# Kernel tuning notes

Measured on AMD Instinct MI355X. Metric: run time of the kernel, lower is better.

## Reference

```python
import jax, jax.numpy as jnp
import numpy as np

B, LAT, HID, N, H = 16, 128, 256, 256, 4
C = HID // H
TAU = 1.0


def setup_inputs() -> dict:
    key = jax.random.key(0)
    ks = jax.random.split(key, 16)
    g = lambda k, shape: (jax.random.normal(k, shape, dtype=jnp.float32) * 0.05)
    u = jax.random.uniform(ks[15], (B, N, N), dtype=jnp.float32, minval=1e-6, maxval=1.0 - 1e-6)
    gumbel = -jnp.log(-jnp.log(u))
    return {
        "x": jax.random.normal(ks[0], (B, LAT), dtype=jnp.float32),
        "W0": g(ks[1], (LAT, HID)), "b0": g(ks[2], (HID,)),
        "W1": g(ks[3], (HID, HID)), "b1": g(ks[4], (HID,)),
        "W2": g(ks[5], (HID, N * HID)), "b2": g(ks[6], (N * HID,)),
        "Wg": g(ks[7], (HID, H * C)),
        "att_src": g(ks[8], (H, C)), "att_dst": g(ks[9], (H, C)),
        "bg": g(ks[10], (H * C,)),
        "Wl": g(ks[11], (HID, N)), "bl": g(ks[12], (N,)),
        "gumbel": gumbel,
    }


def _forward(x, W0, b0, W1, b1, W2, b2, Wg, att_src, att_dst, bg, Wl, bl, gumbel):
    batch = x.shape[0]
    n = bl.shape[0]
    heads, ch = att_src.shape
    hid = heads * ch
    # MLP: latent -> hidden -> hidden -> n_nodes*hidden
    h = jax.nn.relu(x @ W0 + b0)
    h = jax.nn.relu(h @ W1 + b1)
    h = (h @ W2 + b2).reshape(batch, n, hid)
    # edge list: torch.combinations (i<j) directed src->dst, plus PyG self-loops
    s_np, d_np = np.triu_indices(n, k=1)
    src = jnp.concatenate([jnp.asarray(s_np, dtype=jnp.int32), jnp.arange(n, dtype=jnp.int32)])
    dst = jnp.concatenate([jnp.asarray(d_np, dtype=jnp.int32), jnp.arange(n, dtype=jnp.int32)])

    def gat(xn):  # xn: [N, hid]
        gfeat = (xn @ Wg).reshape(n, heads, ch)
        a_s = jnp.einsum('nhc,hc->nh', gfeat, att_src)
        a_d = jnp.einsum('nhc,hc->nh', gfeat, att_dst)
        e = jax.nn.leaky_relu(a_s[src] + a_d[dst], 0.2)          # [E, H]
        m = jax.lax.stop_gradient(jax.ops.segment_max(e, dst, num_segments=n))
        p = jnp.exp(e - m[dst])
        denom = jax.ops.segment_sum(p, dst, num_segments=n)
        alpha = p / denom[dst]                                   # segment softmax per dst
        out = jax.ops.segment_sum(gfeat[src] * alpha[:, :, None], dst, num_segments=n)
        return out.reshape(n, hid) + bg

    h = jax.nn.elu(jax.vmap(gat)(h))  # dropout is a no-op (eval mode)
    logits = h @ Wl + bl
    # gumbel_softmax(hard=True) with straight-through estimator
    y_soft = jax.nn.softmax((logits + gumbel) / TAU, axis=-1)
    y_hard = jax.nn.one_hot(jnp.argmax(y_soft, axis=-1), n, dtype=y_soft.dtype)
    y = jax.lax.stop_gradient(y_hard - y_soft) + y_soft
    adj = jnp.clip(y + jnp.swapaxes(y, 1, 2), 0.0, 1.0)
    return adj


def reference(x, W0, b0, W1, b1, W2, b2, Wg, att_src, att_dst, bg, Wl, bl, gumbel):
    return _forward(x, W0, b0, W1, b1, W2, b2, Wg, att_src, att_dst, bg, Wl, bl, gumbel)
```

## Files before the change

### kernel.cpp

```cpp
#include <hip/hip_runtime.h>
#include <math.h>

#define NB 16
#define LAT 128
#define HID 256
#define NN 256
#define NH 4
#define JT 4

__device__ __forceinline__ float lrelu02(float x){ return x > 0.f ? x : 0.2f*x; }
__device__ __forceinline__ float eluf(float x){ return x > 0.f ? x : expm1f(x); }

__global__ __launch_bounds__(256) void k_mlp12(const float* __restrict__ x,
    const float* __restrict__ W0, const float* __restrict__ b0,
    const float* __restrict__ W1, const float* __restrict__ b1,
    float* __restrict__ h2)
{
    __shared__ float xs[LAT];
    __shared__ float h1s[HID];
    int b = blockIdx.x, t = threadIdx.x;
    if (t < LAT) xs[t] = x[b*LAT + t];
    __syncthreads();
    float acc = b0[t];
    for (int k = 0; k < LAT; ++k) acc = fmaf(xs[k], W0[k*HID + t], acc);
    h1s[t] = fmaxf(acc, 0.f);
    __syncthreads();
    float acc2 = b1[t];
    for (int k = 0; k < HID; ++k) acc2 = fmaf(h1s[k], W1[k*HID + t], acc2);
    h2[b*HID + t] = fmaxf(acc2, 0.f);
}

__global__ __launch_bounds__(512) void k_mlp3g(
    const float* __restrict__ h2, const float* __restrict__ W2,
    const float* __restrict__ b2, const float* __restrict__ Wg,
    const float* __restrict__ att_src, const float* __restrict__ att_dst,
    float* __restrict__ gfeat, float* __restrict__ a_s, float* __restrict__ a_d)
{
    __shared__ float h2T[HID][16];
    __shared__ float red[256*17];
    __shared__ float h3s[NB][HID+1];
    int t = threadIdx.x;
    int n = blockIdx.x;
    int col = t & 255, kh = t >> 8;
    for (int idx = t; idx < NB*HID; idx += 512) {
        int b = idx & 15, k = idx >> 4;
        h2T[k][b] = h2[b*HID + k];
    }
    __syncthreads();
    float acc[NB];
    #pragma unroll
    for (int b = 0; b < NB; ++b) acc[b] = 0.f;
    const float* w2p = W2 + (size_t)kh*128*65536 + (size_t)n*HID + col;
    for (int k0 = 0; k0 < 128; k0 += 16) {
        float wv[16];
        #pragma unroll
        for (int u = 0; u < 16; ++u) wv[u] = w2p[(size_t)(k0+u)*65536];
        #pragma unroll
        for (int u = 0; u < 16; ++u) {
            const float* hr = &h2T[kh*128 + k0 + u][0];
            #pragma unroll
            for (int b = 0; b < NB; ++b) acc[b] = fmaf(hr[b], wv[u], acc[b]);
        }
    }
    if (kh == 1) {
        #pragma unroll
        for (int b = 0; b < NB; ++b) red[col*17 + b] = acc[b];
    }
    __syncthreads();
    if (kh == 0) {
        float bv = b2[n*HID + col];
        #pragma unroll
        for (int b = 0; b < NB; ++b) h3s[b][col] = acc[b] + red[col*17 + b] + bv;
    }
    __syncthreads();
    int l = t & 63, w = t >> 6, cb = l*4;
    float4 g[2];
    g[0] = make_float4(0.f,0.f,0.f,0.f); g[1] = g[0];
    #pragma unroll 4
    for (int k = 0; k < HID; ++k) {
        float4 wg = *(const float4*)&Wg[k*HID + cb];
        #pragma unroll
        for (int rr = 0; rr < 2; ++rr) {
            float hv = h3s[w*2+rr][k];
            g[rr].x = fmaf(hv, wg.x, g[rr].x);
            g[rr].y = fmaf(hv, wg.y, g[rr].y);
            g[rr].z = fmaf(hv, wg.z, g[rr].z);
            g[rr].w = fmaf(hv, wg.w, g[rr].w);
        }
    }
    float4 s4 = *(const float4*)&att_src[cb];
    float4 d4 = *(const float4*)&att_dst[cb];
    int h = l >> 4;
    #pragma unroll
    for (int rr = 0; rr < 2; ++rr) {
        int b = w*2 + rr;
        *(float4*)&gfeat[b*(NN*HID) + n*HID + cb] = g[rr];
        float ps = g[rr].x*s4.x + g[rr].y*s4.y + g[rr].z*s4.z + g[rr].w*s4.w;
        float pd = g[rr].x*d4.x + g[rr].y*d4.y + g[rr].z*d4.z + g[rr].w*d4.w;
        #pragma unroll
        for (int off = 1; off < 16; off <<= 1) {
            ps += __shfl_xor(ps, off);
            pd += __shfl_xor(pd, off);
        }
        if ((l & 15) == 0) {
            a_s[b*(NN*NH) + n*NH + h] = ps;
            a_d[b*(NN*NH) + n*NH + h] = pd;
        }
    }
}

__global__ __launch_bounds__(256) void k_prefden(const float* __restrict__ a_s,
    const float* __restrict__ a_d, float* __restrict__ sArr)
{
    __shared__ float as_sh[NN];
    int id = blockIdx.x;
    int b = id >> 4, h = (id >> 2) & 3, jc = id & 3;
    int t = threadIdx.x;
    as_sh[t] = a_s[b*(NN*NH) + t*NH + h];
    __syncthreads();
    int jl = t >> 2, r = t & 3;
    int j = jc*64 + jl;
    float ad = a_d[b*(NN*NH) + j*NH + h];
    float lm = -INFINITY;
    for (int i = r; i <= j; i += 4) lm = fmaxf(lm, as_sh[i]);
    lm = fmaxf(lm, __shfl_xor(lm, 1));
    lm = fmaxf(lm, __shfl_xor(lm, 2));
    float m = lrelu02(lm + ad);
    float s = 0.f;
    for (int i = r; i <= j; i += 4) s += expf(lrelu02(as_sh[i] + ad) - m);
    s += __shfl_xor(s, 1);
    s += __shfl_xor(s, 2);
    if (r == 0) {
        sArr[b*(NN*NH) + j*NH + h] = expf(-m) / s;
    }
}

__global__ __launch_bounds__(256) void k_gatlog(
    const float* __restrict__ gfeat, const float* __restrict__ a_s,
    const float* __restrict__ a_d, const float* __restrict__ sArr,
    const float* __restrict__ bg, const float* __restrict__ Wl,
    const float* __restrict__ bl, const float* __restrict__ gumbel,
    int* __restrict__ biOut)
{
    __shared__ float pa[4*1032];
    __shared__ float part[16*256];
    __shared__ float houts[NN*4];
    __shared__ float redv[4][JT];
    __shared__ int   redi[4][JT];

    int t = threadIdx.x;
    int id = blockIdx.x;
    int xcd = id & 7, k2 = id >> 3;
    int bb = (xcd << 1) | (k2 >> 6);
    int j0 = (k2 & 63) * JT;
    int l = t & 63, w = t >> 6;

    float pr[JT][4];
    if (w*64 <= j0 + JT - 1) {
        float4 as4 = *(const float4*)&a_s[bb*(NN*NH) + t*NH];
        #pragma unroll
        for (int jj = 0; jj < JT; ++jj) {
            int j = j0 + jj;
            float4 ad4 = *(const float4*)&a_d[bb*(NN*NH) + j*NH];
            float4 sv4 = *(const float4*)&sArr[bb*(NN*NH) + j*NH];
            bool valid = (t <= j);
            pr[jj][0] = valid ? expf(lrelu02(as4.x+ad4.x)) * sv4.x : 0.f;
            pr[jj][1] = valid ? expf(lrelu02(as4.y+ad4.y)) * sv4.y : 0.f;
            pr[jj][2] = valid ? expf(lrelu02(as4.z+ad4.z)) * sv4.z : 0.f;
            pr[jj][3] = valid ? expf(lrelu02(as4.w+ad4.w)) * sv4.w : 0.f;
        }
    } else {
        #pragma unroll
        for (int jj = 0; jj < JT; ++jj)
            #pragma unroll
            for (int h = 0; h < 4; ++h) pr[jj][h] = 0.f;
    }
    #pragma unroll
    for (int h = 0; h < 4; ++h)
        *(float4*)&pa[h*1032 + t*4] = make_float4(pr[0][h], pr[1][h], pr[2][h], pr[3][h]);
    __syncthreads();

    int q = l >> 4, c4 = (l & 15) * 4;
    float4 aj[JT];
    #pragma unroll
    for (int jj = 0; jj < JT; ++jj) aj[jj] = make_float4(0.f,0.f,0.f,0.f);
    const float* gb = gfeat + bb*(NN*HID);
    int lim = j0 + JT - w*64; lim = lim < 0 ? 0 : (lim > 64 ? 64 : lim);
    #pragma unroll 4
    for (int ii = 0; ii < lim; ++ii) {
        int ig = w*64 + ii;
        float4 g4 = *(const float4*)&gb[ig*HID + q*64 + c4];
        float4 pv = *(const float4*)&pa[q*1032 + ig*4];
        aj[0].x = fmaf(pv.x, g4.x, aj[0].x); aj[0].y = fmaf(pv.x, g4.y, aj[0].y);
        aj[0].z = fmaf(pv.x, g4.z, aj[0].z); aj[0].w = fmaf(pv.x, g4.w, aj[0].w);
        aj[1].x = fmaf(pv.y, g4.x, aj[1].x); aj[1].y = fmaf(pv.y, g4.y, aj[1].y);
        aj[1].z = fmaf(pv.y, g4.z, aj[1].z); aj[1].w = fmaf(pv.y, g4.w, aj[1].w);
        aj[2].x = fmaf(pv.z, g4.x, aj[2].x); aj[2].y = fmaf(pv.z, g4.y, aj[2].y);
        aj[2].z = fmaf(pv.z, g4.z, aj[2].z); aj[2].w = fmaf(pv.z, g4.w, aj[2].w);
        aj[3].x = fmaf(pv.w, g4.x, aj[3].x); aj[3].y = fmaf(pv.w, g4.y, aj[3].y);
        aj[3].z = fmaf(pv.w, g4.z, aj[3].z); aj[3].w = fmaf(pv.w, g4.w, aj[3].w);
    }
    #pragma unroll
    for (int jj = 0; jj < JT; ++jj)
        *(float4*)&part[(w*JT + jj)*256 + q*64 + c4] = aj[jj];
    __syncthreads();

    {
        float bgv = bg[t];
        float hh[JT];
        #pragma unroll
        for (int jj = 0; jj < JT; ++jj) {
            float s = part[(0*JT+jj)*256 + t] + part[(1*JT+jj)*256 + t]
                    + part[(2*JT+jj)*256 + t] + part[(3*JT+jj)*256 + t] + bgv;
            hh[jj] = eluf(s);
        }
        *(float4*)&houts[t*4] = make_float4(hh[0], hh[1], hh[2], hh[3]);
    }
    __syncthreads();

    int cb = l*4;
    float4 lg[JT];
    #pragma unroll
    for (int jj = 0; jj < JT; ++jj) lg[jj] = make_float4(0.f,0.f,0.f,0.f);
    #pragma unroll 2
    for (int kk = 0; kk < 64; ++kk) {
        int k = w*64 + kk;
        float4 hv  = *(const float4*)&houts[k*4];
        float4 wl4 = *(const float4*)&Wl[k*HID + cb];
        lg[0].x = fmaf(hv.x, wl4.x, lg[0].x); lg[0].y = fmaf(hv.x, wl4.y, lg[0].y);
        lg[0].z = fmaf(hv.x, wl4.z, lg[0].z); lg[0].w = fmaf(hv.x, wl4.w, lg[0].w);
        lg[1].x = fmaf(hv.y, wl4.x, lg[1].x); lg[1].y = fmaf(hv.y, wl4.y, lg[1].y);
        lg[1].z = fmaf(hv.y, wl4.z, lg[1].z); lg[1].w = fmaf(hv.y, wl4.w, lg[1].w);
        lg[2].x = fmaf(hv.z, wl4.x, lg[2].x); lg[2].y = fmaf(hv.z, wl4.y, lg[2].y);
        lg[2].z = fmaf(hv.z, wl4.z, lg[2].z); lg[2].w = fmaf(hv.z, wl4.w, lg[2].w);
        lg[3].x = fmaf(hv.w, wl4.x, lg[3].x); lg[3].y = fmaf(hv.w, wl4.y, lg[3].y);
        lg[3].z = fmaf(hv.w, wl4.z, lg[3].z); lg[3].w = fmaf(hv.w, wl4.w, lg[3].w);
    }
    #pragma unroll
    for (int jj = 0; jj < JT; ++jj)
        *(float4*)&part[(w*JT + jj)*256 + cb] = lg[jj];
    __syncthreads();

    float blv = bl[t];
    #pragma unroll
    for (int jj = 0; jj < JT; ++jj) {
        float z = part[(0*JT+jj)*256 + t] + part[(1*JT+jj)*256 + t]
                + part[(2*JT+jj)*256 + t] + part[(3*JT+jj)*256 + t]
                + blv + gumbel[bb*(NN*NN) + (j0+jj)*NN + t];
        float bv = z; int bi_ = t;
        #pragma unroll
        for (int off = 1; off < 64; off <<= 1) {
            float ov = __shfl_xor(bv, off);
            int   oi = __shfl_xor(bi_, off);
            if (ov > bv || (ov == bv && oi < bi_)) { bv = ov; bi_ = oi; }
        }
        if (l == 0) { redv[w][jj] = bv; redi[w][jj] = bi_; }
    }
    __syncthreads();
    if (t < JT) {
        float bv = redv[0][t]; int bi_ = redi[0][t];
        #pragma unroll
        for (int ww = 1; ww < 4; ++ww)
            if (redv[ww][t] > bv) { bv = redv[ww][t]; bi_ = redi[ww][t]; }
        biOut[bb*NN + j0 + t] = bi_;
    }
}

__global__ __launch_bounds__(256) void k_adj(const int* __restrict__ bi,
    float* __restrict__ adj)
{
    int bb = blockIdx.x, t = threadIdx.x;
    float4* ap = (float4*)(adj + (size_t)bb*(NN*NN));
    float4 z = make_float4(0.f,0.f,0.f,0.f);
    for (int idx = t; idx < NN*NN/4; idx += 256) ap[idx] = z;
    __syncthreads();
    int b = bi[bb*NN + t];
    adj[(size_t)bb*(NN*NN) + t*NN + b] = 1.0f;
    adj[(size_t)bb*(NN*NN) + b*NN + t] = 1.0f;
}

extern "C" void kernel_launch(void* const* d_in, const int* in_sizes, int n_in,
                              void* d_out, int out_size, void* d_ws, size_t ws_size,
                              hipStream_t stream)
{
    const float* x       = (const float*)d_in[0];
    const float* W0      = (const float*)d_in[1];
    const float* b0      = (const float*)d_in[2];
    const float* W1      = (const float*)d_in[3];
    const float* b1      = (const float*)d_in[4];
    const float* W2      = (const float*)d_in[5];
    const float* b2      = (const float*)d_in[6];
    const float* Wg      = (const float*)d_in[7];
    const float* att_src = (const float*)d_in[8];
    const float* att_dst = (const float*)d_in[9];
    const float* bg      = (const float*)d_in[10];
    const float* Wl      = (const float*)d_in[11];
    const float* bl      = (const float*)d_in[12];
    const float* gumbel  = (const float*)d_in[13];

    float* ws     = (float*)d_ws;
    float* h2     = ws;
    float* a_s    = h2 + 4096;
    float* a_d    = a_s + 16384;
    float* sArr   = a_d + 16384;
    int*   biIdx  = (int*)(sArr + 16384);
    float* gfeat  = (float*)d_out;
    float* adj    = (float*)d_out;

    k_mlp12  <<<NB, 256, 0, stream>>>(x, W0, b0, W1, b1, h2);
    k_mlp3g  <<<NN, 512, 0, stream>>>(h2, W2, b2, Wg, att_src, att_dst, gfeat, a_s, a_d);
    k_prefden<<<256, 256, 0, stream>>>(a_s, a_d, sArr);
    k_gatlog <<<NB*64, 256, 0, stream>>>(gfeat, a_s, a_d, sArr, bg, Wl, bl, gumbel, biIdx);
    k_adj    <<<NB, 256, 0, stream>>>(biIdx, adj);
}
```

Before: 88.86 us.

## Split W2 GEMM into its own wide kernel and compute GAT features in place

The fused MLP-layer-3 plus GAT-projection kernel is split in two. The first, k_h3, runs 1024 blocks of 256 threads, each handling 64 output columns with a four-way K split and double-buffered W2 loads, so the 64 MB W2 stream gets more parallelism and more loads in flight. The second kernel reads h3 back from the output buffer and overwrites each node's slice in place with its GAT features. This adds one extra launch and a global round trip for h3 (about 4 MB) in exchange for better bandwidth use on the dominant W2 read.

```diff
diff --git a/kernel.cpp b/kernel.cpp
--- a/kernel.cpp
+++ b/kernel.cpp
@@ -30,62 +30,93 @@
     h2[b*HID + t] = fmaxf(acc2, 0.f);
 }
 
-__global__ __launch_bounds__(512) void k_mlp3g(
+#define FMA16(KK, WV) do { \
+    const float4* hq = (const float4*)&h2T[KK][0]; \
+    float4 q0 = hq[0], q1 = hq[1], q2 = hq[2], q3 = hq[3]; \
+    acc[0] = fmaf(q0.x,(WV),acc[0]);  acc[1] = fmaf(q0.y,(WV),acc[1]); \
+    acc[2] = fmaf(q0.z,(WV),acc[2]);  acc[3] = fmaf(q0.w,(WV),acc[3]); \
+    acc[4] = fmaf(q1.x,(WV),acc[4]);  acc[5] = fmaf(q1.y,(WV),acc[5]); \
+    acc[6] = fmaf(q1.z,(WV),acc[6]);  acc[7] = fmaf(q1.w,(WV),acc[7]); \
+    acc[8] = fmaf(q2.x,(WV),acc[8]);  acc[9] = fmaf(q2.y,(WV),acc[9]); \
+    acc[10]= fmaf(q2.z,(WV),acc[10]); acc[11]= fmaf(q2.w,(WV),acc[11]); \
+    acc[12]= fmaf(q3.x,(WV),acc[12]); acc[13]= fmaf(q3.y,(WV),acc[13]); \
+    acc[14]= fmaf(q3.z,(WV),acc[14]); acc[15]= fmaf(q3.w,(WV),acc[15]); \
+} while (0)
+
+__global__ __launch_bounds__(256) void k_h3(
     const float* __restrict__ h2, const float* __restrict__ W2,
-    const float* __restrict__ b2, const float* __restrict__ Wg,
+    const float* __restrict__ b2, float* __restrict__ h3)
+{
+    __shared__ float h2T[HID][16];
+    __shared__ float red[3][64][17];
+    int t = threadIdx.x;
+    int c = t & 63, kh = t >> 6;
+    int col = blockIdx.x*64 + c;
+    for (int idx = t; idx < NB*HID; idx += 256) {
+        int b = idx & 15, k = idx >> 4;
+        h2T[k][b] = h2[b*HID + k];
+    }
+    __syncthreads();
+    float acc[16];
+    #pragma unroll
+    for (int b = 0; b < 16; ++b) acc[b] = 0.f;
+    const float* p = W2 + (size_t)(kh*64)*65536 + col;
+    float wa[8], wb[8];
+    #pragma unroll
+    for (int u = 0; u < 8; ++u) wa[u] = p[(size_t)u*65536];
+    for (int k0 = 0; k0 < 64; k0 += 16) {
+        #pragma unroll
+        for (int u = 0; u < 8; ++u) wb[u] = p[(size_t)(k0+8+u)*65536];
+        #pragma unroll
+        for (int u = 0; u < 8; ++u) { int kk = kh*64 + k0 + u; FMA16(kk, wa[u]); }
+        if (k0 + 16 < 64) {
+            #pragma unroll
+            for (int u = 0; u < 8; ++u) wa[u] = p[(size_t)(k0+16+u)*65536];
+        }
+        #pragma unroll
+        for (int u = 0; u < 8; ++u) { int kk = kh*64 + k0 + 8 + u; FMA16(kk, wb[u]); }
+    }
+    if (kh > 0) {
+        #pragma unroll
+        for (int b = 0; b < 16; ++b) red[kh-1][c][b] = acc[b];
+    }
+    __syncthreads();
+    if (kh == 0) {
+        float bv = b2[col];
+        #pragma unroll
+        for (int b = 0; b < 16; ++b) {
+            float s = acc[b] + red[0][c][b] + red[1][c][b] + red[2][c][b] + bv;
+            h3[(size_t)b*65536 + col] = s;
+        }
+    }
+}
+
+__global__ __launch_bounds__(512) void k_gfeatB(
+    float* __restrict__ g, const float* __restrict__ Wg,
     const float* __restrict__ att_src, const float* __restrict__ att_dst,
-    float* __restrict__ gfeat, float* __restrict__ a_s, float* __restrict__ a_d)
-{
-    __shared__ float h2T[HID][16];
-    __shared__ float red[256*17];
+    float* __restrict__ a_s, float* __restrict__ a_d)
+{
     __shared__ float h3s[NB][HID+1];
     int t = threadIdx.x;
     int n = blockIdx.x;
-    int col = t & 255, kh = t >> 8;
     for (int idx = t; idx < NB*HID; idx += 512) {
-        int b = idx & 15, k = idx >> 4;
-        h2T[k][b] = h2[b*HID + k];
-    }
-    __syncthreads();
-    float acc[NB];
-    #pragma unroll
-    for (int b = 0; b < NB; ++b) acc[b] = 0.f;
-    const float* w2p = W2 + (size_t)kh*128*65536 + (size_t)n*HID + col;
-    for (int k0 = 0; k0 < 128; k0 += 16) {
-        float wv[16];
-        #pragma unroll
-        for (int u = 0; u < 16; ++u) wv[u] = w2p[(size_t)(k0+u)*65536];
-        #pragma unroll
-        for (int u = 0; u < 16; ++u) {
-            const float* hr = &h2T[kh*128 + k0 + u][0];
-            #pragma unroll
-            for (int b = 0; b < NB; ++b) acc[b] = fmaf(hr[b], wv[u], acc[b]);
-        }
-    }
-    if (kh == 1) {
-        #pragma unroll
-        for (int b = 0; b < NB; ++b) red[col*17 + b] = acc[b];
-    }
-    __syncthreads();
-    if (kh == 0) {
-        float bv = b2[n*HID + col];
-        #pragma unroll
-        for (int b = 0; b < NB; ++b) h3s[b][col] = acc[b] + red[col*17 + b] + bv;
+        int b = idx >> 8, c = idx & 255;
+        h3s[b][c] = g[(size_t)b*65536 + n*HID + c];
     }
     __syncthreads();
     int l = t & 63, w = t >> 6, cb = l*4;
-    float4 g[2];
-    g[0] = make_float4(0.f,0.f,0.f,0.f); g[1] = g[0];
+    float4 gg[2];
+    gg[0] = make_float4(0.f,0.f,0.f,0.f); gg[1] = gg[0];
     #pragma unroll 4
     for (int k = 0; k < HID; ++k) {
         float4 wg = *(const float4*)&Wg[k*HID + cb];
         #pragma unroll
         for (int rr = 0; rr < 2; ++rr) {
             float hv = h3s[w*2+rr][k];
-            g[rr].x = fmaf(hv, wg.x, g[rr].x);
-            g[rr].y = fmaf(hv, wg.y, g[rr].y);
-            g[rr].z = fmaf(hv, wg.z, g[rr].z);
-            g[rr].w = fmaf(hv, wg.w, g[rr].w);
+            gg[rr].x = fmaf(hv, wg.x, gg[rr].x);
+            gg[rr].y = fmaf(hv, wg.y, gg[rr].y);
+            gg[rr].z = fmaf(hv, wg.z, gg[rr].z);
+            gg[rr].w = fmaf(hv, wg.w, gg[rr].w);
         }
     }
     float4 s4 = *(const float4*)&att_src[cb];
@@ -94,9 +125,9 @@
     #pragma unroll
     for (int rr = 0; rr < 2; ++rr) {
         int b = w*2 + rr;
-        *(float4*)&gfeat[b*(NN*HID) + n*HID + cb] = g[rr];
-        float ps = g[rr].x*s4.x + g[rr].y*s4.y + g[rr].z*s4.z + g[rr].w*s4.w;
-        float pd = g[rr].x*d4.x + g[rr].y*d4.y + g[rr].z*d4.z + g[rr].w*d4.w;
+        *(float4*)&g[(size_t)b*65536 + n*HID + cb] = gg[rr];
+        float ps = gg[rr].x*s4.x + gg[rr].y*s4.y + gg[rr].z*s4.z + gg[rr].w*s4.w;
+        float pd = gg[rr].x*d4.x + gg[rr].y*d4.y + gg[rr].z*d4.z + gg[rr].w*d4.w;
         #pragma unroll
         for (int off = 1; off < 16; off <<= 1) {
             ps += __shfl_xor(ps, off);
@@ -184,12 +215,12 @@
     float4 aj[JT];
     #pragma unroll
     for (int jj = 0; jj < JT; ++jj) aj[jj] = make_float4(0.f,0.f,0.f,0.f);
-    const float* gb = gfeat + bb*(NN*HID);
+    const float* gb = gfeat + (size_t)0;
     int lim = j0 + JT - w*64; lim = lim < 0 ? 0 : (lim > 64 ? 64 : lim);
     #pragma unroll 4
     for (int ii = 0; ii < lim; ++ii) {
         int ig = w*64 + ii;
-        float4 g4 = *(const float4*)&gb[ig*HID + q*64 + c4];
+        float4 g4 = *(const float4*)&gb[(size_t)bb*(NN*HID) + ig*HID + q*64 + c4];
         float4 pv = *(const float4*)&pa[q*1032 + ig*4];
         aj[0].x = fmaf(pv.x, g4.x, aj[0].x); aj[0].y = fmaf(pv.x, g4.y, aj[0].y);
         aj[0].z = fmaf(pv.x, g4.z, aj[0].z); aj[0].w = fmaf(pv.x, g4.w, aj[0].w);
@@ -246,7 +277,7 @@
     for (int jj = 0; jj < JT; ++jj) {
         float z = part[(0*JT+jj)*256 + t] + part[(1*JT+jj)*256 + t]
                 + part[(2*JT+jj)*256 + t] + part[(3*JT+jj)*256 + t]
-                + blv + gumbel[bb*(NN*NN) + (j0+jj)*NN + t];
+                + blv + gumbel[(size_t)bb*(NN*NN) + (j0+jj)*NN + t];
         float bv = z; int bi_ = t;
         #pragma unroll
         for (int off = 1; off < 64; off <<= 1) {
@@ -304,12 +335,13 @@
     float* a_d    = a_s + 16384;
     float* sArr   = a_d + 16384;
     int*   biIdx  = (int*)(sArr + 16384);
-    float* gfeat  = (float*)d_out;
+    float* h3g    = (float*)d_out;
     float* adj    = (float*)d_out;
 
     k_mlp12  <<<NB, 256, 0, stream>>>(x, W0, b0, W1, b1, h2);
-    k_mlp3g  <<<NN, 512, 0, stream>>>(h2, W2, b2, Wg, att_src, att_dst, gfeat, a_s, a_d);
+    k_h3     <<<1024, 256, 0, stream>>>(h2, W2, b2, h3g);
+    k_gfeatB <<<NN, 512, 0, stream>>>(h3g, Wg, att_src, att_dst, a_s, a_d);
     k_prefden<<<256, 256, 0, stream>>>(a_s, a_d, sArr);
-    k_gatlog <<<NB*64, 256, 0, stream>>>(gfeat, a_s, a_d, sArr, bg, Wl, bl, gumbel, biIdx);
+    k_gatlog <<<NB*64, 256, 0, stream>>>(h3g, a_s, a_d, sArr, bg, Wl, bl, gumbel, biIdx);
     k_adj    <<<NB, 256, 0, stream>>>(biIdx, adj);
 }
```

After: 97.96 us. 1.1x slower.

## Restructure W2/Wg GEMM kernel with float4 loads, K-split warps and prefetch

Applied to the files above, without the earlier changes.

Replaces the 512-thread W2 GEMM kernel with a 256-thread version. Each wave now handles a 64-row K slice, each thread loads float4 columns of W2 with register double-buffered prefetch, and partial sums are combined through sequential shared-memory accumulation. The Wg projection also uses prefetched float4 weights and computes 4 batch rows per wave instead of 2. The aim is wider, better-pipelined global loads of the large W2 matrix. In exchange the kernel uses many more registers (64 float4 accumulators) and four serialized barrier rounds for the reduction.

```diff
diff --git a/kernel.cpp b/kernel.cpp
--- a/kernel.cpp
+++ b/kernel.cpp
@@ -30,73 +30,121 @@
     h2[b*HID + t] = fmaxf(acc2, 0.f);
 }
 
-__global__ __launch_bounds__(512) void k_mlp3g(
+#define FMA_B(HB, ACC) \
+    ACC.x = fmaf((HB), wv.x, ACC.x); ACC.y = fmaf((HB), wv.y, ACC.y); \
+    ACC.z = fmaf((HB), wv.z, ACC.z); ACC.w = fmaf((HB), wv.w, ACC.w);
+
+__global__ __launch_bounds__(256, 2) void k_h3g(
     const float* __restrict__ h2, const float* __restrict__ W2,
     const float* __restrict__ b2, const float* __restrict__ Wg,
     const float* __restrict__ att_src, const float* __restrict__ att_dst,
     float* __restrict__ gfeat, float* __restrict__ a_s, float* __restrict__ a_d)
 {
     __shared__ float h2T[HID][16];
-    __shared__ float red[256*17];
-    __shared__ float h3s[NB][HID+1];
+    __shared__ float h3s[NB][HID+4];
     int t = threadIdx.x;
     int n = blockIdx.x;
-    int col = t & 255, kh = t >> 8;
-    for (int idx = t; idx < NB*HID; idx += 512) {
+    int l = t & 63, w = t >> 6;
+    for (int idx = t; idx < NB*HID; idx += 256) {
         int b = idx & 15, k = idx >> 4;
         h2T[k][b] = h2[b*HID + k];
     }
     __syncthreads();
-    float acc[NB];
-    #pragma unroll
-    for (int b = 0; b < NB; ++b) acc[b] = 0.f;
-    const float* w2p = W2 + (size_t)kh*128*65536 + (size_t)n*HID + col;
-    for (int k0 = 0; k0 < 128; k0 += 16) {
-        float wv[16];
-        #pragma unroll
-        for (int u = 0; u < 16; ++u) wv[u] = w2p[(size_t)(k0+u)*65536];
-        #pragma unroll
-        for (int u = 0; u < 16; ++u) {
-            const float* hr = &h2T[kh*128 + k0 + u][0];
-            #pragma unroll
-            for (int b = 0; b < NB; ++b) acc[b] = fmaf(hr[b], wv[u], acc[b]);
-        }
-    }
-    if (kh == 1) {
-        #pragma unroll
-        for (int b = 0; b < NB; ++b) red[col*17 + b] = acc[b];
-    }
-    __syncthreads();
-    if (kh == 0) {
-        float bv = b2[n*HID + col];
-        #pragma unroll
-        for (int b = 0; b < NB; ++b) h3s[b][col] = acc[b] + red[col*17 + b] + bv;
-    }
-    __syncthreads();
-    int l = t & 63, w = t >> 6, cb = l*4;
-    float4 g[2];
-    g[0] = make_float4(0.f,0.f,0.f,0.f); g[1] = g[0];
-    #pragma unroll 4
-    for (int k = 0; k < HID; ++k) {
-        float4 wg = *(const float4*)&Wg[k*HID + cb];
-        #pragma unroll
-        for (int rr = 0; rr < 2; ++rr) {
-            float hv = h3s[w*2+rr][k];
-            g[rr].x = fmaf(hv, wg.x, g[rr].x);
-            g[rr].y = fmaf(hv, wg.y, g[rr].y);
-            g[rr].z = fmaf(hv, wg.z, g[rr].z);
-            g[rr].w = fmaf(hv, wg.w, g[rr].w);
+
+    float4 acc[16];
+    {
+        float4 bq = *(const float4*)&b2[n*HID + l*4];
+        float4 z  = make_float4(0.f,0.f,0.f,0.f);
+        #pragma unroll
+        for (int b = 0; b < 16; ++b) acc[b] = (w == 0) ? bq : z;
+    }
+    {
+        const float* p = W2 + (size_t)(w*64)*65536 + n*HID + l*4;
+        float4 buf[8];
+        #pragma unroll
+        for (int u = 0; u < 8; ++u) buf[u] = *(const float4*)(p + (size_t)u*65536);
+        for (int k0 = 0; k0 < 64; k0 += 8) {
+            #pragma unroll
+            for (int u = 0; u < 8; ++u) {
+                float4 wv = buf[u];
+                if (k0 + 8 < 64)
+                    buf[u] = *(const float4*)(p + (size_t)(k0+8+u)*65536);
+                int k = w*64 + k0 + u;
+                const float4* hq = (const float4*)&h2T[k][0];
+                float4 q0 = hq[0], q1 = hq[1], q2 = hq[2], q3 = hq[3];
+                FMA_B(q0.x, acc[0])  FMA_B(q0.y, acc[1])
+                FMA_B(q0.z, acc[2])  FMA_B(q0.w, acc[3])
+                FMA_B(q1.x, acc[4])  FMA_B(q1.y, acc[5])
+                FMA_B(q1.z, acc[6])  FMA_B(q1.w, acc[7])
+                FMA_B(q2.x, acc[8])  FMA_B(q2.y, acc[9])
+                FMA_B(q2.z, acc[10]) FMA_B(q2.w, acc[11])
+                FMA_B(q3.x, acc[12]) FMA_B(q3.y, acc[13])
+                FMA_B(q3.z, acc[14]) FMA_B(q3.w, acc[15])
+            }
+        }
+    }
+    for (int ww = 0; ww < 4; ++ww) {
+        if (w == ww) {
+            #pragma unroll
+            for (int b = 0; b < 16; ++b) {
+                float4* dst = (float4*)&h3s[b][l*4];
+                if (ww == 0) *dst = acc[b];
+                else {
+                    float4 v = *dst;
+                    v.x += acc[b].x; v.y += acc[b].y;
+                    v.z += acc[b].z; v.w += acc[b].w;
+                    *dst = v;
+                }
+            }
+        }
+        __syncthreads();
+    }
+
+    int cb = l*4;
+    float4 gg[4];
+    #pragma unroll
+    for (int rr = 0; rr < 4; ++rr) gg[rr] = make_float4(0.f,0.f,0.f,0.f);
+    {
+        const float* wp = Wg + cb;
+        float4 wbuf[8];
+        #pragma unroll
+        for (int u = 0; u < 8; ++u) wbuf[u] = *(const float4*)(wp + u*HID);
+        for (int k0 = 0; k0 < HID; k0 += 8) {
+            float4 h4[4][2];
+            #pragma unroll
+            for (int rr = 0; rr < 4; ++rr) {
+                h4[rr][0] = *(const float4*)&h3s[4*w+rr][k0];
+                h4[rr][1] = *(const float4*)&h3s[4*w+rr][k0+4];
+            }
+            #pragma unroll
+            for (int u = 0; u < 8; ++u) {
+                float4 wg = wbuf[u];
+                if (k0 + 8 < HID)
+                    wbuf[u] = *(const float4*)(wp + (k0+8+u)*HID);
+                #pragma unroll
+                for (int rr = 0; rr < 4; ++rr) {
+                    float hv = (u < 4)
+                        ? ((u & 3) == 0 ? h4[rr][0].x : (u & 3) == 1 ? h4[rr][0].y
+                           : (u & 3) == 2 ? h4[rr][0].z : h4[rr][0].w)
+                        : ((u & 3) == 0 ? h4[rr][1].x : (u & 3) == 1 ? h4[rr][1].y
+                           : (u & 3) == 2 ? h4[rr][1].z : h4[rr][1].w);
+                    gg[rr].x = fmaf(hv, wg.x, gg[rr].x);
+                    gg[rr].y = fmaf(hv, wg.y, gg[rr].y);
+                    gg[rr].z = fmaf(hv, wg.z, gg[rr].z);
+                    gg[rr].w = fmaf(hv, wg.w, gg[rr].w);
+                }
+            }
         }
     }
     float4 s4 = *(const float4*)&att_src[cb];
     float4 d4 = *(const float4*)&att_dst[cb];
     int h = l >> 4;
     #pragma unroll
-    for (int rr = 0; rr < 2; ++rr) {
-        int b = w*2 + rr;
-        *(float4*)&gfeat[b*(NN*HID) + n*HID + cb] = g[rr];
-        float ps = g[rr].x*s4.x + g[rr].y*s4.y + g[rr].z*s4.z + g[rr].w*s4.w;
-        float pd = g[rr].x*d4.x + g[rr].y*d4.y + g[rr].z*d4.z + g[rr].w*d4.w;
+    for (int rr = 0; rr < 4; ++rr) {
+        int b = 4*w + rr;
+        *(float4*)&gfeat[(size_t)b*(NN*HID) + n*HID + cb] = gg[rr];
+        float ps = gg[rr].x*s4.x + gg[rr].y*s4.y + gg[rr].z*s4.z + gg[rr].w*s4.w;
+        float pd = gg[rr].x*d4.x + gg[rr].y*d4.y + gg[rr].z*d4.z + gg[rr].w*d4.w;
         #pragma unroll
         for (int off = 1; off < 16; off <<= 1) {
             ps += __shfl_xor(ps, off);
@@ -184,12 +232,11 @@
     float4 aj[JT];
     #pragma unroll
     for (int jj = 0; jj < JT; ++jj) aj[jj] = make_float4(0.f,0.f,0.f,0.f);
-    const float* gb = gfeat + bb*(NN*HID);
     int lim = j0 + JT - w*64; lim = lim < 0 ? 0 : (lim > 64 ? 64 : lim);
     #pragma unroll 4
     for (int ii = 0; ii < lim; ++ii) {
         int ig = w*64 + ii;
-        float4 g4 = *(const float4*)&gb[ig*HID + q*64 + c4];
+        float4 g4 = *(const float4*)&gfeat[(size_t)bb*(NN*HID) + ig*HID + q*64 + c4];
         float4 pv = *(const float4*)&pa[q*1032 + ig*4];
         aj[0].x = fmaf(pv.x, g4.x, aj[0].x); aj[0].y = fmaf(pv.x, g4.y, aj[0].y);
         aj[0].z = fmaf(pv.x, g4.z, aj[0].z); aj[0].w = fmaf(pv.x, g4.w, aj[0].w);
@@ -246,7 +293,7 @@
     for (int jj = 0; jj < JT; ++jj) {
         float z = part[(0*JT+jj)*256 + t] + part[(1*JT+jj)*256 + t]
                 + part[(2*JT+jj)*256 + t] + part[(3*JT+jj)*256 + t]
-                + blv + gumbel[bb*(NN*NN) + (j0+jj)*NN + t];
+                + blv + gumbel[(size_t)bb*(NN*NN) + (j0+jj)*NN + t];
         float bv = z; int bi_ = t;
         #pragma unroll
         for (int off = 1; off < 64; off <<= 1) {
@@ -308,7 +355,7 @@
     float* adj    = (float*)d_out;
 
     k_mlp12  <<<NB, 256, 0, stream>>>(x, W0, b0, W1, b1, h2);
-    k_mlp3g  <<<NN, 512, 0, stream>>>(h2, W2, b2, Wg, att_src, att_dst, gfeat, a_s, a_d);
+    k_h3g    <<<NN, 256, 0, stream>>>(h2, W2, b2, Wg, att_src, att_dst, gfeat, a_s, a_d);
     k_prefden<<<256, 256, 0, stream>>>(a_s, a_d, sArr);
     k_gatlog <<<NB*64, 256, 0, stream>>>(gfeat, a_s, a_d, sArr, bg, Wl, bl, gumbel, biIdx);
     k_adj    <<<NB, 256, 0, stream>>>(biIdx, adj);
```

New measurement: 115.4 us. 1.3x slower.
